# Kernel tuning notes

Hardware: AMD Instinct MI355X
Metric: run time of the kernel (lower is better)

Reference implementation:

```python
import jax, jax.numpy as jnp
import numpy as np

B, L = 2, 160
RD = 128          # residue_dim
AD = 128          # atom_dim
NUM_AT = 37       # atom37
NSC = 34          # side-chain atom slots (37 - 3 backbone)
EPS = 8.0         # radius for eps_8 graph
NOISE = 0.5       # noise added to repeated CA positions
HID = 512         # decoder MLP hidden


def _precomputed_atom37_mask():
    # Stand-in for VALID_ATOM37_MASK [20 residue types, 37 atoms]:
    # backbone N,CA,C,O always present; deterministic pseudo side-chain counts.
    m = np.zeros((20, NUM_AT), np.float32)
    m[:, :4] = 1.0
    for r in range(20):
        nsc = 1 + (r * 7) % 10
        m[r, 4:4 + nsc] = 1.0
    return jnp.asarray(m)


def setup_inputs() -> dict:
    key = jax.random.key(0)
    ks = jax.random.split(key, 8)
    bb_pred = jax.random.normal(ks[0], (B, L, 3, 3), jnp.float32) * 10.0
    scalar_features = jax.random.normal(ks[1], (B, L, RD), jnp.float32)
    aa_pred = jax.random.normal(ks[2], (B, L, 20), jnp.float32)
    mask = jnp.ones((B, L), jnp.float32)
    residue_batch = jnp.repeat(jnp.arange(B, dtype=jnp.int64), L)
    # learned parameters
    atom_emb = jax.random.normal(ks[3], (NUM_AT, AD), jnp.float32) * 0.02
    W1 = jax.random.normal(ks[4], (2 * AD, HID), jnp.float32) / np.sqrt(2.0 * AD)
    b1 = jnp.zeros((HID,), jnp.float32)
    W2 = jax.random.normal(ks[5], (HID, 3), jnp.float32) / np.sqrt(float(HID))
    b2 = jnp.zeros((3,), jnp.float32)
    # pre-sampled position noise (torch.randn_like * noise)
    pos_noise = jax.random.normal(ks[6], (B, L, NSC, 3), jnp.float32) * NOISE
    precomputed_mask = _precomputed_atom37_mask()
    return dict(bb_pred=bb_pred, scalar_features=scalar_features, aa_pred=aa_pred,
                residue_batch=residue_batch, mask=mask, precomputed_mask=precomputed_mask,
                atom_emb=atom_emb, W1=W1, b1=b1, W2=W2, b2=b2, pos_noise=pos_noise)


def reference(bb_pred, scalar_features, aa_pred, residue_batch, mask,
              precomputed_mask, atom_emb, W1, b1, W2, b2, pos_noise):
    # --- generate_atom37_mask ---
    res_types = jnp.argmax(aa_pred, axis=-1)                       # [B,L]
    atom_mask = precomputed_mask[res_types] * mask[..., None]      # [B,L,37]

    # --- ResidueAndAtomEmbedder (dense, validity carried as mask) ---
    atom_type_emb = atom_emb[None, None] * atom_mask[..., None]    # [B,L,37,AD]
    combined = scalar_features[:, :, None, :] + atom_type_emb      # [B,L,37,AD]
    sc_mask = atom_mask[:, :, 3:]                                  # [B,L,34]
    h = combined[:, :, 3:, :] * sc_mask[..., None]                 # [B,L,34,AD]

    # --- reconstruct_edges: CA repeated per side-chain slot + noise ---
    ca = bb_pred[:, :, 1, :] * mask[..., None]                     # [B,L,3]
    pos = ca[:, :, None, :] + pos_noise                            # [B,L,34,3]

    Ns = L * NSC
    x = pos.reshape(B, Ns, 3)
    hf = h.reshape(B, Ns, AD)
    valid = sc_mask.reshape(B, Ns)                                 # batch axis B == residue_batch separation

    # pairwise squared distances [B,Ns,Ns] (eps_8 radius graph, dense masked form)
    x2 = jnp.sum(x * x, axis=-1)
    d2 = x2[:, :, None] + x2[:, None, :] - 2.0 * jnp.einsum('bnd,bmd->bnm', x, x)
    pair_valid = valid[:, :, None] * valid[:, None, :]
    w = jnp.where(d2 < EPS * EPS, jnp.exp(-d2 / (2.0 * EPS * EPS)), 0.0) * pair_valid

    # --- PositionDecoder (EGNN-style layer, self-loops contribute zero rel-pos) ---
    deg = jnp.sum(w, axis=-1, keepdims=True)                       # [B,Ns,1]
    inv = 1.0 / (deg + 1.0)
    agg_pos = (x * deg - jnp.einsum('bnm,bmd->bnd', w, x)) * inv   # sum_j w_ij (x_i - x_j), normalized
    h_agg = jnp.einsum('bnm,bmd->bnd', w, hf) * inv                # [B,Ns,AD]
    z = jnp.concatenate([hf, h_agg], axis=-1)                      # [B,Ns,2*AD]
    gate = jnp.tanh(jax.nn.relu(z @ W1 + b1) @ W2 + b2)            # [B,Ns,3]
    disp = agg_pos * gate * valid[..., None]

    updated_pos = (x + disp).reshape(B, L, NSC, 3)
    return atom_mask, updated_pos
```

## Files before the change

kernel.cpp:

```cpp
#include <hip/hip_runtime.h>
#include <hip/hip_bf16.h>
#include <math.h>

#define BB 2
#define LL 160
#define NSC 34
#define NS (LL * NSC)
#define TOT (BB * NS)
#define AD 128
#define ADX 144
#define HID 512
#define NAT 37
#define KC 8
#define NVP 1792
#define NVT 28
#define NVPT (BB * NVP)
#define PEN 1.0e9f

typedef __attribute__((ext_vector_type(4))) float f32x4;
typedef __attribute__((ext_vector_type(8))) short s16x8;
typedef __attribute__((address_space(1))) const unsigned int gu32;
typedef __attribute__((address_space(3))) unsigned int lu32;

__global__ __launch_bounds__(256) void k_pre(
    const float* __restrict__ W1, __hip_bfloat16* __restrict__ W1T,
    const float* __restrict__ bb, const float* __restrict__ aa,
    const float* __restrict__ mask, const float* __restrict__ pm,
    const float* __restrict__ noise,
    float* __restrict__ out_mask, float4* __restrict__ ws_xe,
    float* __restrict__ ws_val, float* __restrict__ out_pos) {
  __shared__ float t[64][65];
  int blk = blockIdx.x;
  int tid = threadIdx.x;
  if (blk < 32) {
    int j0 = (blk >> 2) * 64;
    int c0 = (blk & 3) * 64;
    for (int i = tid; i < 64 * 64; i += 256) {
      int jl = i & 63, cl = i >> 6;
      t[cl][jl] = W1[(size_t)(c0 + cl) * HID + j0 + jl];
    }
    __syncthreads();
    for (int i = tid; i < 64 * 64; i += 256) {
      int cl = i & 63, jl = i >> 6;
      W1T[(size_t)(j0 + jl) * 256 + c0 + cl] = __float2bfloat16(t[cl][jl]);
    }
    return;
  }
  int bl = blk - 32;
  int b = bl / LL, l = bl % LL;
  const float* ap = aa + bl * 20;
  float mv = ap[0]; int rt = 0;
  for (int r = 1; r < 20; ++r) { float v = ap[r]; if (v > mv) { mv = v; rt = r; } }
  float mk = mask[bl];
  const float* pmr = pm + rt * NAT;
  if (tid < NAT) out_mask[bl * NAT + tid] = pmr[tid] * mk;

  float ca0 = bb[(bl * 3 + 1) * 3 + 0] * mk;
  float ca1 = bb[(bl * 3 + 1) * 3 + 1] * mk;
  float ca2 = bb[(bl * 3 + 1) * 3 + 2] * mk;

  if (tid < NSC) {
    float am = pmr[3 + tid] * mk;
    const float* npz = noise + (bl * NSC + tid) * 3;
    float x = ca0 + npz[0], y = ca1 + npz[1], z = ca2 + npz[2];
    float4 xv;
    xv.x = x; xv.y = y; xv.z = z;
    xv.w = x * x + y * y + z * z + (am > 0.f ? 0.f : PEN);
    int g = b * NS + l * NSC + tid;
    ws_xe[g] = xv;
    ws_val[g] = am;
  }
  if (tid < NSC * 3) {
    int s = tid / 3, c = tid % 3;
    float ca = (c == 0) ? ca0 : (c == 1) ? ca1 : ca2;
    float pos = ca + noise[(bl * NSC + s) * 3 + c];
    out_pos[(size_t)(b * NS + l * NSC + s) * 3 + c] = pos;
  }
}

__global__ __launch_bounds__(256) void k_prep1c(
    const float* __restrict__ sf, const float* __restrict__ emb,
    const float* __restrict__ ws_val, const float4* __restrict__ ws_xe,
    int* __restrict__ cg2g, float4* __restrict__ xc,
    __hip_bfloat16* __restrict__ hfTc, __hip_bfloat16* __restrict__ ws_z) {
  __shared__ int sincl[256];
  __shared__ int smap[NVP];
  __shared__ __hip_bfloat16 tile[ADX][64];
  int bid = blockIdx.x;
  int b = bid / NVT;
  int j0 = (bid % NVT) * 64;
  int tid = threadIdx.x;

  int c = 0;
  if (tid < LL) {
    for (int s = 0; s < NSC; ++s)
      if (ws_val[b * NS + tid * NSC + s] > 0.f) ++c;
  }
  sincl[tid] = c;
  __syncthreads();
  #pragma unroll
  for (int off = 1; off < 256; off <<= 1) {
    int t = (tid >= off) ? sincl[tid - off] : 0;
    __syncthreads();
    sincl[tid] += t;
    __syncthreads();
  }
  for (int j = tid; j < NVP; j += 256) smap[j] = -1;
  __syncthreads();
  if (tid < LL) {
    int o = sincl[tid] - c, k = 0;
    for (int s = 0; s < NSC; ++s) {
      int m = tid * NSC + s;
      if (ws_val[b * NS + m] > 0.f) { smap[o + k] = m; ++k; }
    }
  }
  __syncthreads();

  if (tid < 64) {
    int j = j0 + tid;
    int m = smap[j];
    cg2g[b * NVP + j] = m;
    float4 v;
    if (m >= 0) v = ws_xe[b * NS + m];
    else { v.x = 0.f; v.y = 0.f; v.z = 0.f; v.w = PEN; }
    xc[b * NVP + j] = v;
  }

  int jl = tid >> 2, cq = tid & 3;
  int m = smap[j0 + jl];
  union { s16x8 v[4]; __hip_bfloat16 h[32]; } o;
  if (m >= 0) {
    int l = m / NSC, s = m - l * NSC;
    float am = ws_val[b * NS + m];
    const float* sfp = sf + (size_t)(b * LL + l) * AD + cq * 32;
    const float* emp = emb + (size_t)(3 + s) * AD + cq * 32;
    #pragma unroll 8
    for (int k = 0; k < 32; ++k) {
      float hv = (sfp[k] + emp[k] * am) * am;
      o.h[k] = __float2bfloat16(hv);
      tile[cq * 32 + k][jl] = o.h[k];
    }
  } else {
    __hip_bfloat16 zz = __float2bfloat16(0.0f);
    #pragma unroll 8
    for (int k = 0; k < 32; ++k) { o.h[k] = zz; tile[cq * 32 + k][jl] = zz; }
  }
  {
    __hip_bfloat16* zp = ws_z + ((size_t)(b * NVP + j0 + jl)) * 128 + cq * 32;
    #pragma unroll
    for (int q = 0; q < 4; ++q) *(s16x8*)(zp + q * 8) = o.v[q];
  }
  if (cq == 0) {
    float xjx = 0.f, xjy = 0.f, xjz = 0.f;
    if (m >= 0) {
      float4 xj = ws_xe[b * NS + m];
      xjx = xj.x; xjy = xj.y; xjz = xj.z;
    }
    tile[128][jl] = __float2bfloat16(m >= 0 ? 1.0f : 0.0f);
    tile[129][jl] = __float2bfloat16(xjx);
    tile[130][jl] = __float2bfloat16(xjy);
    tile[131][jl] = __float2bfloat16(xjz);
    __hip_bfloat16 zz = __float2bfloat16(0.0f);
    for (int rr = 132; rr < ADX; ++rr) tile[rr][jl] = zz;
  }
  __syncthreads();
  for (int i = tid; i < ADX * 2; i += 256) {
    int r = i >> 1, hf = i & 1;
    __hip_bfloat16* dst = hfTc + (size_t)b * ADX * NVP + (size_t)r * NVP + j0 + hf * 32;
    const __hip_bfloat16* srow = &tile[r][hf * 32];
    #pragma unroll
    for (int q = 0; q < 4; ++q)
      *(s16x8*)(dst + q * 8) = *(const s16x8*)(srow + q * 8);
  }
}

__global__ __launch_bounds__(256, 4) void k_haggc(
    const float4* __restrict__ xc, const __hip_bfloat16* __restrict__ hfTc,
    __hip_bfloat16* __restrict__ haggp, float* __restrict__ dgp) {
  constexpr int NSTEP = NVP / 32;
  constexpr int CH_MAX = (NSTEP + KC - 1) / KC;
  __shared__ float4 xs[(CH_MAX * 4 + 1) * 9];
  __shared__ alignas(16) __hip_bfloat16 sB[2][4608];

  int bid = blockIdx.x;
  int b = bid / (NVT * KC);
  int rem = bid % (NVT * KC);
  int kc = rem / NVT;
  int nt = rem % NVT;
  int n0 = nt * 64;
  int sb = (kc * NSTEP) / KC, se = ((kc + 1) * NSTEP) / KC;
  int tid = threadIdx.x, w = tid >> 6, lane = tid & 63;
  int ln = lane & 15, g8 = (lane >> 4) * 8;

  const float4* xb = xc + b * NVP;
  const __hip_bfloat16* hb = hfTc + (size_t)b * ADX * NVP;

  int mcnt = (se - sb) * 32;
  for (int i = tid; i < mcnt; i += 256)
    xs[(i >> 3) * 9 + (i & 7)] = xb[sb * 32 + i];

  float4 xn = xb[n0 + w * 16 + ln];
  float x2n = xn.w;

  f32x4 acc[9];
  #pragma unroll
  for (int ct = 0; ct < 9; ++ct) acc[ct] = (f32x4){0.f, 0.f, 0.f, 0.f};

  auto STAGE = [&](int s, int pb) {
    const char* srcb = (const char*)(hb + (size_t)s * 32);
    #pragma unroll
    for (int k = 0; k < 3; ++k) {
      int t = tid + k * 256;
      if (t < 576) {
        int row = t >> 2;
        int sl = (t & 3) ^ (row & 3);
        const gu32* gp = (const gu32*)(const void*)(srcb + (size_t)row * (NVP * 2) + sl * 16);
        lu32* lp = (lu32*)(void*)((char*)&sB[pb][0] + (size_t)(t & ~63) * 16);
        __builtin_amdgcn_global_load_lds(gp, lp, 16, 0, 0);
      }
    }
  };

  STAGE(sb, 0);
  __syncthreads();

  int cur = 0;
  for (int s = sb; s < se; ++s) {
    if (s + 1 < se) STAGE(s + 1, cur ^ 1);
    int grp = (s - sb) * 4 + (g8 >> 3);
    union { s16x8 v; __hip_bfloat16 h[8]; } af;
    #pragma unroll
    for (int j = 0; j < 8; ++j) {
      float4 xm = xs[grp * 9 + j];
      float dt = xn.x * xm.x + xn.y * xm.y + xn.z * xm.z;
      float d2 = x2n + xm.w - 2.f * dt;
      float wv = (d2 < 64.f) ? __expf(d2 * -0.0078125f) : 0.f;
      af.h[j] = __float2bfloat16(wv);
    }
    const char* bbase = (const char*)&sB[cur][0];
    int slot = g8 >> 3;
    #pragma unroll
    for (int ct = 0; ct < 9; ++ct) {
      int row = ct * 16 + ln;
      int boff = (row << 6) + ((slot ^ (row & 3)) << 4);
      s16x8 bf = *(const s16x8*)(bbase + boff);
      acc[ct] = __builtin_amdgcn_mfma_f32_16x16x32_bf16(af.v, bf, acc[ct], 0, 0, 0);
    }
    __syncthreads();
    cur ^= 1;
  }

  int q = lane >> 4;
  int grow = b * NVP + n0 + w * 16 + q * 4;
  #pragma unroll
  for (int ct = 0; ct < 8; ++ct)
    #pragma unroll
    for (int r = 0; r < 4; ++r)
      haggp[((size_t)kc * NVPT + grow + r) * AD + ct * 16 + ln] = __float2bfloat16(acc[ct][r]);
  if (ln < 4)
    #pragma unroll
    for (int r = 0; r < 4; ++r)
      dgp[((size_t)kc * NVPT + grow + r) * 4 + ln] = acc[8][r];
}

__global__ __launch_bounds__(512) void k_mlpf(
    const __hip_bfloat16* __restrict__ ws_z,
    const __hip_bfloat16* __restrict__ haggp, const float* __restrict__ dgp,
    const __hip_bfloat16* __restrict__ W1T, const float* __restrict__ b1v,
    const float* __restrict__ W2, const float* __restrict__ b2v,
    const float4* __restrict__ xc, const int* __restrict__ cg2g,
    const float* __restrict__ ws_val, float* __restrict__ out_pos) {
  __shared__ __hip_bfloat16 zt[32][136];
  __shared__ float sai[32][4];
  __shared__ float ppart[4][32][3];

  int r0 = blockIdx.x * 32;
  int tid = threadIdx.x, w = tid >> 6, lane = tid & 63;
  int ln = lane & 15, g8 = (lane >> 4) * 8, q = lane >> 4;
  int rowhalf = w & 1, js4 = w >> 1;

  if (tid < 32) {
    int g = r0 + tid;
    float deg = 0.f, wx = 0.f, wy = 0.f, wz = 0.f;
    #pragma unroll
    for (int kc = 0; kc < KC; ++kc) {
      float4 d = *(const float4*)&dgp[((size_t)kc * NVPT + g) * 4];
      deg += d.x; wx += d.y; wy += d.z; wz += d.w;
    }
    float inv = 1.f / (deg + 1.f);
    float4 xv = xc[g];
    sai[tid][0] = (xv.x * deg - wx) * inv;
    sai[tid][1] = (xv.y * deg - wy) * inv;
    sai[tid][2] = (xv.z * deg - wz) * inv;
    sai[tid][3] = inv;
  }
  __syncthreads();
  {
    int row = tid >> 4, c8 = tid & 15;
    int g = r0 + row;
    float s[8];
    #pragma unroll
    for (int j = 0; j < 8; ++j) s[j] = 0.f;
    #pragma unroll
    for (int kc = 0; kc < KC; ++kc) {
      union { s16x8 v; __hip_bfloat16 h[8]; } uu;
      uu.v = *(const s16x8*)(haggp + ((size_t)kc * NVPT + g) * AD + c8 * 8);
      #pragma unroll
      for (int j = 0; j < 8; ++j) s[j] += __bfloat162float(uu.h[j]);
    }
    float inv = sai[row][3];
    #pragma unroll
    for (int j = 0; j < 8; ++j)
      zt[row][c8 * 8 + j] = __float2bfloat16(s[j] * inv);
  }
  __syncthreads();

  int arl = rowhalf * 16 + ln;
  int arow = r0 + arl;
  s16x8 a[8];
  #pragma unroll
  for (int kq = 0; kq < 4; ++kq)
    a[kq] = *(const s16x8*)(ws_z + (size_t)arow * 128 + kq * 32 + g8);
  #pragma unroll
  for (int kq = 4; kq < 8; ++kq)
    a[kq] = *(const s16x8*)&zt[arl][(kq - 4) * 32 + g8];

  float p[4][3];
  #pragma unroll
  for (int r = 0; r < 4; ++r)
    #pragma unroll
    for (int o = 0; o < 3; ++o) p[r][o] = 0.f;

  #pragma unroll
  for (int jt = 0; jt < 8; ++jt) {
    int j = js4 * 128 + jt * 16 + ln;
    f32x4 acc = (f32x4){0.f, 0.f, 0.f, 0.f};
    #pragma unroll
    for (int kq = 0; kq < 8; ++kq) {
      s16x8 bw = *(const s16x8*)(W1T + (size_t)j * 256 + kq * 32 + g8);
      acc = __builtin_amdgcn_mfma_f32_16x16x32_bf16(a[kq], bw, acc, 0, 0, 0);
    }
    float bias = b1v[j];
    float w20 = W2[j * 3 + 0], w21 = W2[j * 3 + 1], w22 = W2[j * 3 + 2];
    #pragma unroll
    for (int r = 0; r < 4; ++r) {
      float h = fmaxf(acc[r] + bias, 0.f);
      p[r][0] += h * w20; p[r][1] += h * w21; p[r][2] += h * w22;
    }
  }
  #pragma unroll
  for (int r = 0; r < 4; ++r)
    #pragma unroll
    for (int o = 0; o < 3; ++o) {
      p[r][o] += __shfl_xor(p[r][o], 1);
      p[r][o] += __shfl_xor(p[r][o], 2);
      p[r][o] += __shfl_xor(p[r][o], 4);
      p[r][o] += __shfl_xor(p[r][o], 8);
    }
  if (ln == 0) {
    #pragma unroll
    for (int r = 0; r < 4; ++r) {
      int row = rowhalf * 16 + q * 4 + r;
      #pragma unroll
      for (int o = 0; o < 3; ++o) ppart[js4][row][o] = p[r][o];
    }
  }
  __syncthreads();

  if (tid < 32) {
    int row = tid;
    int g = r0 + row;
    int bq = g / NVP;
    int m = cg2g[g];
    if (m >= 0) {
      float p0 = b2v[0] + ppart[0][row][0] + ppart[1][row][0] + ppart[2][row][0] + ppart[3][row][0];
      float p1 = b2v[1] + ppart[0][row][1] + ppart[1][row][1] + ppart[2][row][1] + ppart[3][row][1];
      float p2 = b2v[2] + ppart[0][row][2] + ppart[1][row][2] + ppart[2][row][2] + ppart[3][row][2];
      float val = ws_val[bq * NS + m];
      float4 xv = xc[g];
      float* op = out_pos + (size_t)(bq * NS + m) * 3;
      op[0] = xv.x + sai[row][0] * tanhf(p0) * val;
      op[1] = xv.y + sai[row][1] * tanhf(p1) * val;
      op[2] = xv.z + sai[row][2] * tanhf(p2) * val;
    }
  }
}

extern "C" void kernel_launch(void* const* d_in, const int* in_sizes, int n_in,
                              void* d_out, int out_size, void* d_ws, size_t ws_size,
                              hipStream_t stream) {
  const float* bb    = (const float*)d_in[0];
  const float* sf    = (const float*)d_in[1];
  const float* aa    = (const float*)d_in[2];
  const float* mask  = (const float*)d_in[4];
  const float* pm    = (const float*)d_in[5];
  const float* emb   = (const float*)d_in[6];
  const float* W1    = (const float*)d_in[7];
  const float* b1v   = (const float*)d_in[8];
  const float* W2    = (const float*)d_in[9];
  const float* b2v   = (const float*)d_in[10];
  const float* noise = (const float*)d_in[11];

  float* out_mask = (float*)d_out;
  float* out_pos  = (float*)d_out + BB * LL * NAT;

  char* cur = (char*)d_ws;
  auto alloc = [&](size_t bytes) -> char* {
    char* p = cur;
    cur += (bytes + 255) & ~(size_t)255;
    return p;
  };
  float4* ws_xe  = (float4*)alloc((size_t)TOT * 16);
  float*  ws_val = (float*)alloc((size_t)TOT * 4);
  int*    cg2g   = (int*)alloc((size_t)BB * NVP * 4);
  float4* xc     = (float4*)alloc((size_t)BB * NVP * 16);
  float*  ws_dgp = (float*)alloc((size_t)KC * NVPT * 16);
  __hip_bfloat16* ws_w1t = (__hip_bfloat16*)alloc((size_t)HID * 256 * 2);
  __hip_bfloat16* hfTc   = (__hip_bfloat16*)alloc((size_t)BB * ADX * NVP * 2);
  __hip_bfloat16* haggp  = (__hip_bfloat16*)alloc((size_t)KC * NVPT * AD * 2);
  __hip_bfloat16* ws_z   = (__hip_bfloat16*)alloc((size_t)NVPT * 128 * 2);

  hipLaunchKernelGGL(k_pre, dim3(32 + BB * LL), dim3(256), 0, stream,
                     W1, ws_w1t, bb, aa, mask, pm, noise,
                     out_mask, ws_xe, ws_val, out_pos);
  hipLaunchKernelGGL(k_prep1c, dim3(BB * NVT), dim3(256), 0, stream,
                     sf, emb, ws_val, ws_xe, cg2g, xc, hfTc, ws_z);
  hipLaunchKernelGGL(k_haggc, dim3(BB * NVT * KC), dim3(256), 0, stream,
                     xc, hfTc, haggp, ws_dgp);
  hipLaunchKernelGGL(k_mlpf, dim3(NVPT / 32), dim3(512), 0, stream,
                     ws_z, haggp, ws_dgp, ws_w1t, b1v, W2, b2v,
                     xc, cg2g, ws_val, out_pos);
}
```

Measured before the change: 53.75 us.

## Merge prep kernels and skip compute beyond actual valid atom count

Fuses the two preprocessing kernels into one launch: the compaction blocks recompute argmax, mask and positions themselves instead of reading an intermediate buffer, which removes one launch and one global round trip. Each batch's valid side-chain count is written to workspace. The aggregation and MLP kernels then exit early for tiles past that count and trim their reduction loop to it, avoiding work on padded slots. The cost is redundant argmax work per compaction block and some reliance on the padding beyond the valid count staying untouched.

```diff
diff --git a/kernel.cpp b/kernel.cpp
--- a/kernel.cpp
+++ b/kernel.cpp
@@ -22,128 +22,146 @@
 typedef __attribute__((address_space(1))) const unsigned int gu32;
 typedef __attribute__((address_space(3))) unsigned int lu32;
 
-__global__ __launch_bounds__(256) void k_pre(
-    const float* __restrict__ W1, __hip_bfloat16* __restrict__ W1T,
-    const float* __restrict__ bb, const float* __restrict__ aa,
-    const float* __restrict__ mask, const float* __restrict__ pm,
-    const float* __restrict__ noise,
-    float* __restrict__ out_mask, float4* __restrict__ ws_xe,
-    float* __restrict__ ws_val, float* __restrict__ out_pos) {
-  __shared__ float t[64][65];
+struct LdsW { float t[64][65]; };
+struct LdsPC {
+  int sincl[256];
+  int smap[NVP];
+  short srt[LL];
+  float smk[LL];
+  float4 sxc[64];
+  __hip_bfloat16 tile[ADX][64];
+};
+
+__global__ __launch_bounds__(256) void k_prep(
+    const float* __restrict__ W1, const float* __restrict__ bb,
+    const float* __restrict__ aa, const float* __restrict__ mask,
+    const float* __restrict__ pm, const float* __restrict__ noise,
+    const float* __restrict__ sf, const float* __restrict__ emb,
+    float* __restrict__ out_mask, float* __restrict__ out_pos,
+    __hip_bfloat16* __restrict__ W1T, float* __restrict__ ws_val,
+    int* __restrict__ cg2g, float4* __restrict__ xc,
+    __hip_bfloat16* __restrict__ hfTc, __hip_bfloat16* __restrict__ ws_z,
+    int* __restrict__ ws_nv) {
+  __shared__ union { LdsW w; LdsPC c; } u;
   int blk = blockIdx.x;
   int tid = threadIdx.x;
+
   if (blk < 32) {
     int j0 = (blk >> 2) * 64;
     int c0 = (blk & 3) * 64;
     for (int i = tid; i < 64 * 64; i += 256) {
       int jl = i & 63, cl = i >> 6;
-      t[cl][jl] = W1[(size_t)(c0 + cl) * HID + j0 + jl];
+      u.w.t[cl][jl] = W1[(size_t)(c0 + cl) * HID + j0 + jl];
     }
     __syncthreads();
     for (int i = tid; i < 64 * 64; i += 256) {
       int cl = i & 63, jl = i >> 6;
-      W1T[(size_t)(j0 + jl) * 256 + c0 + cl] = __float2bfloat16(t[cl][jl]);
+      W1T[(size_t)(j0 + jl) * 256 + c0 + cl] = __float2bfloat16(u.w.t[cl][jl]);
     }
     return;
   }
-  int bl = blk - 32;
-  int b = bl / LL, l = bl % LL;
-  const float* ap = aa + bl * 20;
-  float mv = ap[0]; int rt = 0;
-  for (int r = 1; r < 20; ++r) { float v = ap[r]; if (v > mv) { mv = v; rt = r; } }
-  float mk = mask[bl];
-  const float* pmr = pm + rt * NAT;
-  if (tid < NAT) out_mask[bl * NAT + tid] = pmr[tid] * mk;
-
-  float ca0 = bb[(bl * 3 + 1) * 3 + 0] * mk;
-  float ca1 = bb[(bl * 3 + 1) * 3 + 1] * mk;
-  float ca2 = bb[(bl * 3 + 1) * 3 + 2] * mk;
-
-  if (tid < NSC) {
-    float am = pmr[3 + tid] * mk;
-    const float* npz = noise + (bl * NSC + tid) * 3;
-    float x = ca0 + npz[0], y = ca1 + npz[1], z = ca2 + npz[2];
-    float4 xv;
-    xv.x = x; xv.y = y; xv.z = z;
-    xv.w = x * x + y * y + z * z + (am > 0.f ? 0.f : PEN);
-    int g = b * NS + l * NSC + tid;
-    ws_xe[g] = xv;
-    ws_val[g] = am;
-  }
-  if (tid < NSC * 3) {
-    int s = tid / 3, c = tid % 3;
-    float ca = (c == 0) ? ca0 : (c == 1) ? ca1 : ca2;
-    float pos = ca + noise[(bl * NSC + s) * 3 + c];
-    out_pos[(size_t)(b * NS + l * NSC + s) * 3 + c] = pos;
-  }
-}
-
-__global__ __launch_bounds__(256) void k_prep1c(
-    const float* __restrict__ sf, const float* __restrict__ emb,
-    const float* __restrict__ ws_val, const float4* __restrict__ ws_xe,
-    int* __restrict__ cg2g, float4* __restrict__ xc,
-    __hip_bfloat16* __restrict__ hfTc, __hip_bfloat16* __restrict__ ws_z) {
-  __shared__ int sincl[256];
-  __shared__ int smap[NVP];
-  __shared__ __hip_bfloat16 tile[ADX][64];
-  int bid = blockIdx.x;
-  int b = bid / NVT;
-  int j0 = (bid % NVT) * 64;
-  int tid = threadIdx.x;
+
+  if (blk < 32 + BB * LL) {
+    int bl = blk - 32;
+    int b = bl / LL, l = bl % LL;
+    const float* ap = aa + bl * 20;
+    float mv = ap[0]; int rt = 0;
+    for (int r = 1; r < 20; ++r) { float v = ap[r]; if (v > mv) { mv = v; rt = r; } }
+    float mk = mask[bl];
+    const float* pmr = pm + rt * NAT;
+    if (tid < NAT) out_mask[bl * NAT + tid] = pmr[tid] * mk;
+    if (tid < NSC) ws_val[b * NS + l * NSC + tid] = pmr[3 + tid] * mk;
+    float ca0 = bb[(bl * 3 + 1) * 3 + 0] * mk;
+    float ca1 = bb[(bl * 3 + 1) * 3 + 1] * mk;
+    float ca2 = bb[(bl * 3 + 1) * 3 + 2] * mk;
+    if (tid < NSC * 3) {
+      int s = tid / 3, c = tid % 3;
+      float ca = (c == 0) ? ca0 : (c == 1) ? ca1 : ca2;
+      out_pos[(size_t)(b * NS + l * NSC + s) * 3 + c] = ca + noise[(bl * NSC + s) * 3 + c];
+    }
+    return;
+  }
+
+  int pb = blk - (32 + BB * LL);
+  int b = pb / NVT;
+  int j0 = (pb % NVT) * 64;
 
   int c = 0;
   if (tid < LL) {
+    int bl = b * LL + tid;
+    const float* ap = aa + bl * 20;
+    float mv = ap[0]; int rt = 0;
+    for (int r = 1; r < 20; ++r) { float v = ap[r]; if (v > mv) { mv = v; rt = r; } }
+    float mk = mask[bl];
+    u.c.srt[tid] = (short)rt;
+    u.c.smk[tid] = mk;
+    const float* pmr = pm + rt * NAT + 3;
     for (int s = 0; s < NSC; ++s)
-      if (ws_val[b * NS + tid * NSC + s] > 0.f) ++c;
-  }
-  sincl[tid] = c;
+      if (pmr[s] * mk > 0.f) ++c;
+  }
+  u.c.sincl[tid] = c;
   __syncthreads();
   #pragma unroll
   for (int off = 1; off < 256; off <<= 1) {
-    int t = (tid >= off) ? sincl[tid - off] : 0;
+    int t = (tid >= off) ? u.c.sincl[tid - off] : 0;
     __syncthreads();
-    sincl[tid] += t;
+    u.c.sincl[tid] += t;
     __syncthreads();
   }
-  for (int j = tid; j < NVP; j += 256) smap[j] = -1;
+  if (tid == 0 && j0 == 0) ws_nv[b] = u.c.sincl[LL - 1];
+  for (int j = tid; j < NVP; j += 256) u.c.smap[j] = -1;
   __syncthreads();
   if (tid < LL) {
-    int o = sincl[tid] - c, k = 0;
+    int o = u.c.sincl[tid] - c, k = 0;
+    const float* pmr = pm + (int)u.c.srt[tid] * NAT + 3;
+    float mk = u.c.smk[tid];
     for (int s = 0; s < NSC; ++s) {
-      int m = tid * NSC + s;
-      if (ws_val[b * NS + m] > 0.f) { smap[o + k] = m; ++k; }
+      if (pmr[s] * mk > 0.f) { u.c.smap[o + k] = tid * NSC + s; ++k; }
     }
   }
   __syncthreads();
 
   if (tid < 64) {
     int j = j0 + tid;
-    int m = smap[j];
+    int m = u.c.smap[j];
     cg2g[b * NVP + j] = m;
     float4 v;
-    if (m >= 0) v = ws_xe[b * NS + m];
-    else { v.x = 0.f; v.y = 0.f; v.z = 0.f; v.w = PEN; }
+    if (m >= 0) {
+      int l = m / NSC, s = m - l * NSC;
+      float mk = u.c.smk[l];
+      int bl = b * LL + l;
+      const float* npz = noise + (bl * NSC + s) * 3;
+      float x = bb[(bl * 3 + 1) * 3 + 0] * mk + npz[0];
+      float y = bb[(bl * 3 + 1) * 3 + 1] * mk + npz[1];
+      float z = bb[(bl * 3 + 1) * 3 + 2] * mk + npz[2];
+      v.x = x; v.y = y; v.z = z;
+      v.w = x * x + y * y + z * z;
+    } else {
+      v.x = 0.f; v.y = 0.f; v.z = 0.f; v.w = PEN;
+    }
     xc[b * NVP + j] = v;
-  }
+    u.c.sxc[tid] = v;
+  }
+  __syncthreads();
 
   int jl = tid >> 2, cq = tid & 3;
-  int m = smap[j0 + jl];
+  int m = u.c.smap[j0 + jl];
   union { s16x8 v[4]; __hip_bfloat16 h[32]; } o;
   if (m >= 0) {
     int l = m / NSC, s = m - l * NSC;
-    float am = ws_val[b * NS + m];
+    float am = pm[(int)u.c.srt[l] * NAT + 3 + s] * u.c.smk[l];
     const float* sfp = sf + (size_t)(b * LL + l) * AD + cq * 32;
     const float* emp = emb + (size_t)(3 + s) * AD + cq * 32;
     #pragma unroll 8
     for (int k = 0; k < 32; ++k) {
       float hv = (sfp[k] + emp[k] * am) * am;
       o.h[k] = __float2bfloat16(hv);
-      tile[cq * 32 + k][jl] = o.h[k];
+      u.c.tile[cq * 32 + k][jl] = o.h[k];
     }
   } else {
     __hip_bfloat16 zz = __float2bfloat16(0.0f);
     #pragma unroll 8
-    for (int k = 0; k < 32; ++k) { o.h[k] = zz; tile[cq * 32 + k][jl] = zz; }
+    for (int k = 0; k < 32; ++k) { o.h[k] = zz; u.c.tile[cq * 32 + k][jl] = zz; }
   }
   {
     __hip_bfloat16* zp = ws_z + ((size_t)(b * NVP + j0 + jl)) * 128 + cq * 32;
@@ -151,23 +169,19 @@
     for (int q = 0; q < 4; ++q) *(s16x8*)(zp + q * 8) = o.v[q];
   }
   if (cq == 0) {
-    float xjx = 0.f, xjy = 0.f, xjz = 0.f;
-    if (m >= 0) {
-      float4 xj = ws_xe[b * NS + m];
-      xjx = xj.x; xjy = xj.y; xjz = xj.z;
-    }
-    tile[128][jl] = __float2bfloat16(m >= 0 ? 1.0f : 0.0f);
-    tile[129][jl] = __float2bfloat16(xjx);
-    tile[130][jl] = __float2bfloat16(xjy);
-    tile[131][jl] = __float2bfloat16(xjz);
+    float4 xj = u.c.sxc[jl];
+    u.c.tile[128][jl] = __float2bfloat16(m >= 0 ? 1.0f : 0.0f);
+    u.c.tile[129][jl] = __float2bfloat16(m >= 0 ? xj.x : 0.f);
+    u.c.tile[130][jl] = __float2bfloat16(m >= 0 ? xj.y : 0.f);
+    u.c.tile[131][jl] = __float2bfloat16(m >= 0 ? xj.z : 0.f);
     __hip_bfloat16 zz = __float2bfloat16(0.0f);
-    for (int rr = 132; rr < ADX; ++rr) tile[rr][jl] = zz;
+    for (int rr = 132; rr < ADX; ++rr) u.c.tile[rr][jl] = zz;
   }
   __syncthreads();
   for (int i = tid; i < ADX * 2; i += 256) {
     int r = i >> 1, hf = i & 1;
     __hip_bfloat16* dst = hfTc + (size_t)b * ADX * NVP + (size_t)r * NVP + j0 + hf * 32;
-    const __hip_bfloat16* srow = &tile[r][hf * 32];
+    const __hip_bfloat16* srow = &u.c.tile[r][hf * 32];
     #pragma unroll
     for (int q = 0; q < 4; ++q)
       *(s16x8*)(dst + q * 8) = *(const s16x8*)(srow + q * 8);
@@ -176,7 +190,8 @@
 
 __global__ __launch_bounds__(256, 4) void k_haggc(
     const float4* __restrict__ xc, const __hip_bfloat16* __restrict__ hfTc,
-    __hip_bfloat16* __restrict__ haggp, float* __restrict__ dgp) {
+    __hip_bfloat16* __restrict__ haggp, float* __restrict__ dgp,
+    const int* __restrict__ ws_nv) {
   constexpr int NSTEP = NVP / 32;
   constexpr int CH_MAX = (NSTEP + KC - 1) / KC;
   __shared__ float4 xs[(CH_MAX * 4 + 1) * 9];
@@ -188,16 +203,16 @@
   int kc = rem / NVT;
   int nt = rem % NVT;
   int n0 = nt * 64;
+  int nv = ws_nv[b];
+  if (n0 >= nv) return;
   int sb = (kc * NSTEP) / KC, se = ((kc + 1) * NSTEP) / KC;
+  int nstep_eff = (nv + 31) >> 5;
+  int se2 = se < nstep_eff ? se : nstep_eff;
   int tid = threadIdx.x, w = tid >> 6, lane = tid & 63;
   int ln = lane & 15, g8 = (lane >> 4) * 8;
 
   const float4* xb = xc + b * NVP;
   const __hip_bfloat16* hb = hfTc + (size_t)b * ADX * NVP;
-
-  int mcnt = (se - sb) * 32;
-  for (int i = tid; i < mcnt; i += 256)
-    xs[(i >> 3) * 9 + (i & 7)] = xb[sb * 32 + i];
 
   float4 xn = xb[n0 + w * 16 + ln];
   float x2n = xn.w;
@@ -221,33 +236,39 @@
     }
   };
 
-  STAGE(sb, 0);
-  __syncthreads();
-
-  int cur = 0;
-  for (int s = sb; s < se; ++s) {
-    if (s + 1 < se) STAGE(s + 1, cur ^ 1);
-    int grp = (s - sb) * 4 + (g8 >> 3);
-    union { s16x8 v; __hip_bfloat16 h[8]; } af;
-    #pragma unroll
-    for (int j = 0; j < 8; ++j) {
-      float4 xm = xs[grp * 9 + j];
-      float dt = xn.x * xm.x + xn.y * xm.y + xn.z * xm.z;
-      float d2 = x2n + xm.w - 2.f * dt;
-      float wv = (d2 < 64.f) ? __expf(d2 * -0.0078125f) : 0.f;
-      af.h[j] = __float2bfloat16(wv);
-    }
-    const char* bbase = (const char*)&sB[cur][0];
-    int slot = g8 >> 3;
-    #pragma unroll
-    for (int ct = 0; ct < 9; ++ct) {
-      int row = ct * 16 + ln;
-      int boff = (row << 6) + ((slot ^ (row & 3)) << 4);
-      s16x8 bf = *(const s16x8*)(bbase + boff);
-      acc[ct] = __builtin_amdgcn_mfma_f32_16x16x32_bf16(af.v, bf, acc[ct], 0, 0, 0);
-    }
+  if (sb < se2) {
+    int mcnt = (se2 - sb) * 32;
+    for (int i = tid; i < mcnt; i += 256)
+      xs[(i >> 3) * 9 + (i & 7)] = xb[sb * 32 + i];
+
+    STAGE(sb, 0);
     __syncthreads();
-    cur ^= 1;
+
+    int cur = 0;
+    for (int s = sb; s < se2; ++s) {
+      if (s + 1 < se2) STAGE(s + 1, cur ^ 1);
+      int grp = (s - sb) * 4 + (g8 >> 3);
+      union { s16x8 v; __hip_bfloat16 h[8]; } af;
+      #pragma unroll
+      for (int j = 0; j < 8; ++j) {
+        float4 xm = xs[grp * 9 + j];
+        float dt = xn.x * xm.x + xn.y * xm.y + xn.z * xm.z;
+        float d2 = x2n + xm.w - 2.f * dt;
+        float wv = (d2 < 64.f) ? __expf(d2 * -0.0078125f) : 0.f;
+        af.h[j] = __float2bfloat16(wv);
+      }
+      const char* bbase = (const char*)&sB[cur][0];
+      int slot = g8 >> 3;
+      #pragma unroll
+      for (int ct = 0; ct < 9; ++ct) {
+        int row = ct * 16 + ln;
+        int boff = (row << 6) + ((slot ^ (row & 3)) << 4);
+        s16x8 bf = *(const s16x8*)(bbase + boff);
+        acc[ct] = __builtin_amdgcn_mfma_f32_16x16x32_bf16(af.v, bf, acc[ct], 0, 0, 0);
+      }
+      __syncthreads();
+      cur ^= 1;
+    }
   }
 
   int q = lane >> 4;
@@ -269,12 +290,16 @@
     const __hip_bfloat16* __restrict__ W1T, const float* __restrict__ b1v,
     const float* __restrict__ W2, const float* __restrict__ b2v,
     const float4* __restrict__ xc, const int* __restrict__ cg2g,
-    const float* __restrict__ ws_val, float* __restrict__ out_pos) {
+    const float* __restrict__ ws_val, float* __restrict__ out_pos,
+    const int* __restrict__ ws_nv) {
   __shared__ __hip_bfloat16 zt[32][136];
   __shared__ float sai[32][4];
   __shared__ float ppart[4][32][3];
 
   int r0 = blockIdx.x * 32;
+  int bq0 = r0 / NVP;
+  if (r0 - bq0 * NVP >= ws_nv[bq0]) return;
+
   int tid = threadIdx.x, w = tid >> 6, lane = tid & 63;
   int ln = lane & 15, g8 = (lane >> 4) * 8, q = lane >> 4;
   int rowhalf = w & 1, js4 = w >> 1;
@@ -410,7 +435,7 @@
     cur += (bytes + 255) & ~(size_t)255;
     return p;
   };
-  float4* ws_xe  = (float4*)alloc((size_t)TOT * 16);
+  int*    ws_nv  = (int*)alloc((size_t)BB * 4);
   float*  ws_val = (float*)alloc((size_t)TOT * 4);
   int*    cg2g   = (int*)alloc((size_t)BB * NVP * 4);
   float4* xc     = (float4*)alloc((size_t)BB * NVP * 16);
@@ -420,14 +445,12 @@
   __hip_bfloat16* haggp  = (__hip_bfloat16*)alloc((size_t)KC * NVPT * AD * 2);
   __hip_bfloat16* ws_z   = (__hip_bfloat16*)alloc((size_t)NVPT * 128 * 2);
 
-  hipLaunchKernelGGL(k_pre, dim3(32 + BB * LL), dim3(256), 0, stream,
-                     W1, ws_w1t, bb, aa, mask, pm, noise,
-                     out_mask, ws_xe, ws_val, out_pos);
-  hipLaunchKernelGGL(k_prep1c, dim3(BB * NVT), dim3(256), 0, stream,
-                     sf, emb, ws_val, ws_xe, cg2g, xc, hfTc, ws_z);
+  hipLaunchKernelGGL(k_prep, dim3(32 + BB * LL + BB * NVT), dim3(256), 0, stream,
+                     W1, bb, aa, mask, pm, noise, sf, emb,
+                     out_mask, out_pos, ws_w1t, ws_val, cg2g, xc, hfTc, ws_z, ws_nv);
   hipLaunchKernelGGL(k_haggc, dim3(BB * NVT * KC), dim3(256), 0, stream,
-                     xc, hfTc, haggp, ws_dgp);
+                     xc, hfTc, haggp, ws_dgp, ws_nv);
   hipLaunchKernelGGL(k_mlpf, dim3(NVPT / 32), dim3(512), 0, stream,
                      ws_z, haggp, ws_dgp, ws_w1t, b1v, W2, b2v,
-                     xc, cg2g, ws_val, out_pos);
+                     xc, cg2g, ws_val, out_pos, ws_nv);
 }
```

Measured after the change: 47.26 us. 12.1% less time.
